# Optimization experiments

Measured on AMD Instinct MI355X. Metric: run time of the kernel, lower is better.

## Reference

```python
import jax, jax.numpy as jnp
import numpy as np

EPS = 1e-8
D = 1024      # embedding_dim
NH = 4        # num_heads
HD = D // NH  # head_dim
B, S = 4, 2048


def setup_inputs() -> dict:
    key = jax.random.key(0)
    k1, k2 = jax.random.split(key)
    x = jax.random.normal(k1, (B, S, 4 * D), dtype=jnp.float32)
    # small-init std = sqrt(2/(5*head_dim)) as in reset_parameters
    std = float(np.sqrt(2.0 / (5.0 * HD)))
    gate_weights = jax.random.normal(k2, (4, NH, HD, HD), dtype=jnp.float32) * std
    # biases: z,i,o zero; f gets powerlaw init (block 0 of 1 -> exponent 0.3)
    term = jnp.arange(HD, dtype=jnp.float32) / (HD - 1.0)
    f_bias = -(-5.0 + 12.0 * term ** 0.3)  # [HD]
    gate_biases = jnp.zeros((4, NH, HD), dtype=jnp.float32)
    gate_biases = gate_biases.at[2].set(jnp.broadcast_to(f_bias, (NH, HD)))
    return {"x_gate_inputs": x, "gate_weights": gate_weights, "gate_biases": gate_biases}


def _slstm_forward(x, W, biases):
    Bn, Sn, _ = x.shape
    # split into 4 gate pre-activations and apply headwise linear per gate
    xg = x.reshape(Bn, Sn, 4, NH, HD)           # gate order z,i,f,o along axis 2
    xg = jnp.moveaxis(xg, 2, 0)                  # [4,B,S,NH,HD]
    # headwise projection: einsum over head-in dim, per gate g and head h
    gates = jnp.einsum('gbshi,ghoi->gbsho', xg, W) + biases[:, None, None]  # [4,B,S,NH,HD]
    gates = jnp.moveaxis(gates, 2, 0)            # [S,4,B,NH,HD] for scan over time

    h0 = jnp.zeros((Bn, NH, HD), dtype=x.dtype)
    carry0 = (h0, h0, h0, jnp.zeros((Bn, NH, HD), dtype=jnp.float32))

    def step(carry, g_t):
        h, c, n, m = carry
        z_b, i_b, f_b, o_b = g_t[0], g_t[1], g_t[2], g_t[3]
        z_val = jnp.tanh(z_b)
        o_val = jax.nn.sigmoid(o_b)
        # faithful to original: exp then log(.+EPS), in m-state dtype (fp32)
        log_f = jnp.log(jnp.exp(f_b).astype(jnp.float32) + EPS)
        log_i = jnp.log(jnp.exp(i_b).astype(jnp.float32) + EPS)
        m_new = jnp.maximum(log_f + m, log_i)
        i_hat = jnp.exp(log_i - m_new).astype(x.dtype)
        f_hat = jnp.exp(log_f + m - m_new).astype(x.dtype)
        c_new = f_hat * c + i_hat * z_val
        n_new = f_hat * n + i_hat
        h_new = o_val * (c_new / (n_new + EPS))
        return (h_new, c_new, n_new, m_new), h_new

    (h_f, c_f, n_f, m_f), hs = jax.lax.scan(step, carry0, gates)
    h_seq = jnp.moveaxis(hs, 0, 1)               # [B,S,NH,HD]
    return h_seq, (h_f, c_f, n_f, m_f)


def reference(x_gate_inputs, gate_weights, gate_biases):
    h_seq, (h_f, c_f, n_f, m_f) = _slstm_forward(x_gate_inputs, gate_weights, gate_biases)
    return h_seq, h_f, c_f, n_f, m_f
```

## Files before the change

kernel.cpp:

```cpp
#include <hip/hip_runtime.h>
#include <cstdint>

#define S_LEN   2048
#define BATCH   4
#define NCH     4096
#define CHUNK   32
#define NCHUNK  64
#define PLANE   ((size_t)S_LEN * NCH)
#define SN      ((size_t)NCHUNK * NCH)
#define EPS     1e-8f

using bf16x8 = __attribute__((ext_vector_type(8))) short;
using u16x8  = __attribute__((ext_vector_type(8))) unsigned short;
using f32x4  = __attribute__((ext_vector_type(4))) float;
typedef unsigned short u16;

__device__ __forceinline__ short f2bf(float f) {
  uint32_t u = __builtin_bit_cast(uint32_t, f);
  u += 0x7fffu + ((u >> 16) & 1u);
  return (short)(u >> 16);
}
__device__ __forceinline__ float bf2f(u16 u) {
  return __builtin_bit_cast(float, (uint32_t)u << 16);
}
__device__ __forceinline__ u16 f2h(float f) {
  _Float16 h = (_Float16)f;
  return __builtin_bit_cast(unsigned short, h);
}
__device__ __forceinline__ float h2f(u16 u) {
  return (float)__builtin_bit_cast(_Float16, u);
}


__global__ __launch_bounds__(1024) void gates_gemm7(
    const float* __restrict__ x, const float* __restrict__ W,
    const float* __restrict__ bias,
    u16* __restrict__ gz16, u16* __restrict__ gi16, u16* __restrict__ gf16,
    u16* __restrict__ go16) {
  __shared__ u16 As[2][16 * 264];

  const int gh  = blockIdx.x;
  const int rg  = blockIdx.y;
  const int g   = gh >> 2, hh = gh & 3;
  const int tid = threadIdx.x;
  const int wave = tid >> 6, lane = tid & 63;
  const int l16 = lane & 15, quad = lane >> 4;
  const int n0  = wave * 16;
  const int row0 = rg * 256;

  bf16x8 Bf[8];
  {
    const float* wp = W + ((size_t)gh << 16) + (n0 + l16) * 256 + quad * 8;
#pragma unroll
    for (int kt = 0; kt < 8; ++kt) {
      float4 w0 = *(const float4*)(wp + kt * 32);
      float4 w1 = *(const float4*)(wp + kt * 32 + 4);
      bf16x8 b;
      b[0] = f2bf(w0.x); b[1] = f2bf(w0.y); b[2] = f2bf(w0.z); b[3] = f2bf(w0.w);
      b[4] = f2bf(w1.x); b[5] = f2bf(w1.y); b[6] = f2bf(w1.z); b[7] = f2bf(w1.w);
      Bf[kt] = b;
    }
  }
  const float bv = bias[gh * 256 + n0 + l16];

  const int sr = tid >> 6, sc = tid & 63;
  const float* sbase = x + (size_t)(row0 + sr) * 4096 + g * 1024 + hh * 256 + sc * 4;

  float4 sreg;
  auto gload = [&](int t) { sreg = *(const float4*)(sbase + (size_t)t * 16 * 4096); };
  auto swrite = [&](int buf) {
    ushort4 u;
    u.x = (u16)f2bf(sreg.x); u.y = (u16)f2bf(sreg.y);
    u.z = (u16)f2bf(sreg.z); u.w = (u16)f2bf(sreg.w);
    *(ushort4*)&As[buf][sr * 264 + sc * 4] = u;
  };

  gload(0); swrite(0);
  __syncthreads();

  for (int t = 0; t < 16; ++t) {
    if (t + 1 < 16) gload(t + 1);

    f32x4 acc = (f32x4){0.f, 0.f, 0.f, 0.f};
#pragma unroll
    for (int kt = 0; kt < 8; ++kt) {
      bf16x8 a = *(const bf16x8*)&As[t & 1][l16 * 264 + kt * 32 + quad * 8];
      acc = __builtin_amdgcn_mfma_f32_16x16x32_bf16(a, Bf[kt], acc, 0, 0, 0);
    }

    {
      int rowb = row0 + t * 16 + quad * 4;
      int sx   = rowb & (S_LEN - 1);
      int bx   = rowb >> 11;
      int ck   = sx >> 5, sin = sx & 31;
      int ch   = bx * 1024 + hh * 256 + n0 + l16;
      size_t idx = ((size_t)ck * NCH + ch) * CHUNK + sin;

      float v0 = acc[0] + bv, v1 = acc[1] + bv, v2 = acc[2] + bv, v3 = acc[3] + bv;
      ushort4 uo;
      if (g == 1) {
        uo.x = f2h(v0); uo.y = f2h(v1); uo.z = f2h(v2); uo.w = f2h(v3);
        *(ushort4*)&gi16[idx] = uo;
      } else if (g == 2) {
        uo.x = f2h(v0); uo.y = f2h(v1); uo.z = f2h(v2); uo.w = f2h(v3);
        *(ushort4*)&gf16[idx] = uo;
      } else if (g == 0) {
        auto tz = [](float v) {
          return (u16)f2bf(1.f - 2.f * __builtin_amdgcn_rcpf(1.f + __expf(2.f * v)));
        };
        uo.x = tz(v0); uo.y = tz(v1); uo.z = tz(v2); uo.w = tz(v3);
        *(ushort4*)&gz16[idx] = uo;
      } else {
        auto sg = [](float v) {
          return (u16)f2bf(__builtin_amdgcn_rcpf(1.f + __expf(-v)));
        };
        uo.x = sg(v0); uo.y = sg(v1); uo.z = sg(v2); uo.w = sg(v3);
        *(ushort4*)&go16[idx] = uo;
      }
    }

    if (t + 1 < 16) {
      swrite((t + 1) & 1);
      __syncthreads();
    }
  }
}

__global__ __launch_bounds__(256) void scan_pass1(
    const u16* __restrict__ gz16, const u16* __restrict__ gi16,
    const u16* __restrict__ gf16, float* __restrict__ sums) {
  const int t  = blockIdx.x * 256 + threadIdx.x;
  const int ch = t & (NCH - 1);
  const int ck = t >> 12;
  const size_t cb = ((size_t)ck * NCH + ch) * CHUNK;

  u16x8 zv[4], iv[4], fv[4];
#pragma unroll
  for (int q = 0; q < 4; ++q) zv[q] = *(const u16x8*)(gz16 + cb + q * 8);
#pragma unroll
  for (int q = 0; q < 4; ++q) iv[q] = *(const u16x8*)(gi16 + cb + q * 8);
#pragma unroll
  for (int q = 0; q < 4; ++q) fv[q] = *(const u16x8*)(gf16 + cb + q * 8);

  float A = 0.f, Bv = -1e30f, D = 0.f, Dn = 0.f;

  auto step = [&](float z, float i, float f) {
    float Bn = fmaxf(Bv + f, i);
    float e1 = __expf(Bv + f - Bn);
    float e2 = __expf(i - Bn);
    D  = e1 * D + e2 * z;
    Dn = e1 * Dn + e2;
    A += f;
    Bv = Bn;
  };

#pragma unroll
  for (int q = 0; q < 4; ++q)
#pragma unroll
    for (int j = 0; j < 8; ++j)
      step(bf2f(zv[q][j]), h2f(iv[q][j]), h2f(fv[q][j]));

  const size_t idx = (size_t)ck * NCH + ch;
  sums[idx]          = A;
  sums[SN + idx]     = Bv;
  sums[2 * SN + idx] = D;
  sums[3 * SN + idx] = Dn;
}

__global__ __launch_bounds__(256) void scan_pass2(
    const float* __restrict__ sums, float* __restrict__ ent) {
  const int gt   = blockIdx.x * 256 + threadIdx.x;
  const int ch   = gt >> 6;
  const int lane = gt & 63;

  const size_t idx = (size_t)lane * NCH + ch;
  float A = sums[idx];
  float B = sums[SN + idx];
  float D = sums[2 * SN + idx];
  float N = sums[3 * SN + idx];

#pragma unroll
  for (int d = 1; d < 64; d <<= 1) {
    float A1 = __shfl_up(A, d, 64);
    float B1 = __shfl_up(B, d, 64);
    float D1 = __shfl_up(D, d, 64);
    float N1 = __shfl_up(N, d, 64);
    if (lane >= d) {
      float Bn = fmaxf(B1 + A, B);
      float e1 = __expf(B1 + A - Bn);
      float e2 = __expf(B - Bn);
      D = e1 * D1 + e2 * D;
      N = e1 * N1 + e2 * N;
      A = A + A1;
      B = Bn;
    }
  }

  float Ae = __shfl_up(A, 1, 64);
  float Be = __shfl_up(B, 1, 64);
  float De = __shfl_up(D, 1, 64);
  float Ne = __shfl_up(N, 1, 64);

  float c, n, m;
  if (lane == 0) {
    c = 0.f; n = 0.f; m = 0.f;
  } else {
    m = fmaxf(Ae, Be);
    float eb = __expf(Be - m);
    c = eb * De;
    n = eb * Ne;
  }

  ent[idx]          = c;
  ent[SN + idx]     = n;
  ent[2 * SN + idx] = m;
}

__global__ __launch_bounds__(256) void scan_pass3(
    const u16* __restrict__ gz16, const u16* __restrict__ gi16,
    const u16* __restrict__ gf16, const u16* __restrict__ go16,
    const float* __restrict__ ent, float* __restrict__ out) {
  const int t  = blockIdx.x * 256 + threadIdx.x;
  const int ch = t & (NCH - 1);
  const int ck = t >> 12;
  const size_t cb = ((size_t)ck * NCH + ch) * CHUNK;

  u16x8 zv[4], iv[4], fv[4], ov[4];
#pragma unroll
  for (int q = 0; q < 4; ++q) zv[q] = *(const u16x8*)(gz16 + cb + q * 8);
#pragma unroll
  for (int q = 0; q < 4; ++q) iv[q] = *(const u16x8*)(gi16 + cb + q * 8);
#pragma unroll
  for (int q = 0; q < 4; ++q) fv[q] = *(const u16x8*)(gf16 + cb + q * 8);
#pragma unroll
  for (int q = 0; q < 4; ++q) ov[q] = *(const u16x8*)(go16 + cb + q * 8);

  const size_t idx0 = (size_t)ck * NCH + ch;
  float c = ent[idx0];
  float n = ent[SN + idx0];
  float m = ent[2 * SN + idx0];

  const int b = ch >> 10, d = ch & 1023;
  float* hout = out + (size_t)b * (S_LEN * 1024) + (size_t)(ck * CHUNK) * 1024 + d;

  float hv = 0.f;
#pragma unroll
  for (int q = 0; q < 4; ++q) {
#pragma unroll
    for (int j = 0; j < 8; ++j) {
      float z = bf2f(zv[q][j]);
      float i = h2f(iv[q][j]);
      float f = h2f(fv[q][j]);
      float o = bf2f(ov[q][j]);
      float mn = fmaxf(f + m, i);
      float fh = __expf(f + m - mn);
      float ih = __expf(i - mn);
      c = fh * c + ih * z;
      n = fh * n + ih;
      m = mn;
      hv = o * c * __builtin_amdgcn_rcpf(n + EPS);
      hout[(size_t)(q * 8 + j) * 1024] = hv;
    }
  }

  if (ck == NCHUNK - 1) {
    float* fin = out + (size_t)BATCH * S_LEN * 1024;
    fin[ch]            = hv;
    fin[NCH + ch]      = c;
    fin[2 * NCH + ch]  = n;
    fin[3 * NCH + ch]  = m;
  }
}

extern "C" void kernel_launch(void* const* d_in, const int* in_sizes, int n_in,
                              void* d_out, int out_size, void* d_ws, size_t ws_size,
                              hipStream_t stream) {
  const float* x    = (const float*)d_in[0];
  const float* W    = (const float*)d_in[1];
  const float* bias = (const float*)d_in[2];
  float* out = (float*)d_out;

  u16*   gz16 = (u16*)d_ws;
  u16*   gi16 = gz16 + PLANE;
  u16*   gf16 = gi16 + PLANE;
  u16*   go16 = gf16 + PLANE;
  float* sums = (float*)(go16 + PLANE);
  float* ent  = sums + 4 * SN;

  gates_gemm7<<<dim3(16, 32), dim3(1024), 0, stream>>>(x, W, bias, gz16, gi16, gf16, go16);
  scan_pass1<<<dim3(1024), dim3(256), 0, stream>>>(gz16, gi16, gf16, sums);
  scan_pass2<<<dim3(1024), dim3(256), 0, stream>>>(sums, ent);
  scan_pass3<<<dim3(1024), dim3(256), 0, stream>>>(gz16, gi16, gf16, go16, ent, out);
}
```

Before: 274.7 us.

## Fuse three-pass chunked scan into one kernel using shared memory

Merges the three scan kernels (chunk reduce, cross-chunk prefix, chunk apply) into a single kernel. Each 1024-thread block owns 16 channels across all 64 chunks and passes chunk summaries through shared memory instead of global workspace. This removes two launches, the global round-trips for sums and entry states, and the reload of z/i/f gates, which now stay in registers. The trade-off is a lower block count (256 blocks of 1024 threads), so more registers are live per thread and occupancy may drop. The global loads in the first phase also become strided, since 16 channels times 64 B each fall within one slot.

```diff
diff --git a/kernel.cpp b/kernel.cpp
--- a/kernel.cpp
+++ b/kernel.cpp
@@ -7,7 +7,6 @@
 #define CHUNK   32
 #define NCHUNK  64
 #define PLANE   ((size_t)S_LEN * NCH)
-#define SN      ((size_t)NCHUNK * NCH)
 #define EPS     1e-8f
 
 using bf16x8 = __attribute__((ext_vector_type(8))) short;
@@ -126,149 +125,137 @@
   }
 }
 
-__global__ __launch_bounds__(256) void scan_pass1(
-    const u16* __restrict__ gz16, const u16* __restrict__ gi16,
-    const u16* __restrict__ gf16, float* __restrict__ sums) {
-  const int t  = blockIdx.x * 256 + threadIdx.x;
-  const int ch = t & (NCH - 1);
-  const int ck = t >> 12;
-  const size_t cb = ((size_t)ck * NCH + ch) * CHUNK;
-
-  u16x8 zv[4], iv[4], fv[4];
-#pragma unroll
-  for (int q = 0; q < 4; ++q) zv[q] = *(const u16x8*)(gz16 + cb + q * 8);
-#pragma unroll
-  for (int q = 0; q < 4; ++q) iv[q] = *(const u16x8*)(gi16 + cb + q * 8);
-#pragma unroll
-  for (int q = 0; q < 4; ++q) fv[q] = *(const u16x8*)(gf16 + cb + q * 8);
-
-  float A = 0.f, Bv = -1e30f, D = 0.f, Dn = 0.f;
-
-  auto step = [&](float z, float i, float f) {
-    float Bn = fmaxf(Bv + f, i);
-    float e1 = __expf(Bv + f - Bn);
-    float e2 = __expf(i - Bn);
-    D  = e1 * D + e2 * z;
-    Dn = e1 * Dn + e2;
-    A += f;
-    Bv = Bn;
-  };
-
-#pragma unroll
-  for (int q = 0; q < 4; ++q)
-#pragma unroll
-    for (int j = 0; j < 8; ++j)
-      step(bf2f(zv[q][j]), h2f(iv[q][j]), h2f(fv[q][j]));
-
-  const size_t idx = (size_t)ck * NCH + ch;
-  sums[idx]          = A;
-  sums[SN + idx]     = Bv;
-  sums[2 * SN + idx] = D;
-  sums[3 * SN + idx] = Dn;
-}
-
-__global__ __launch_bounds__(256) void scan_pass2(
-    const float* __restrict__ sums, float* __restrict__ ent) {
-  const int gt   = blockIdx.x * 256 + threadIdx.x;
-  const int ch   = gt >> 6;
-  const int lane = gt & 63;
-
-  const size_t idx = (size_t)lane * NCH + ch;
-  float A = sums[idx];
-  float B = sums[SN + idx];
-  float D = sums[2 * SN + idx];
-  float N = sums[3 * SN + idx];
-
-#pragma unroll
-  for (int d = 1; d < 64; d <<= 1) {
-    float A1 = __shfl_up(A, d, 64);
-    float B1 = __shfl_up(B, d, 64);
-    float D1 = __shfl_up(D, d, 64);
-    float N1 = __shfl_up(N, d, 64);
-    if (lane >= d) {
-      float Bn = fmaxf(B1 + A, B);
-      float e1 = __expf(B1 + A - Bn);
-      float e2 = __expf(B - Bn);
-      D = e1 * D1 + e2 * D;
-      N = e1 * N1 + e2 * N;
-      A = A + A1;
-      B = Bn;
-    }
-  }
-
-  float Ae = __shfl_up(A, 1, 64);
-  float Be = __shfl_up(B, 1, 64);
-  float De = __shfl_up(D, 1, 64);
-  float Ne = __shfl_up(N, 1, 64);
-
-  float c, n, m;
-  if (lane == 0) {
-    c = 0.f; n = 0.f; m = 0.f;
-  } else {
-    m = fmaxf(Ae, Be);
-    float eb = __expf(Be - m);
-    c = eb * De;
-    n = eb * Ne;
-  }
-
-  ent[idx]          = c;
-  ent[SN + idx]     = n;
-  ent[2 * SN + idx] = m;
-}
-
-__global__ __launch_bounds__(256) void scan_pass3(
+__global__ __launch_bounds__(1024) void scan_fused(
     const u16* __restrict__ gz16, const u16* __restrict__ gi16,
     const u16* __restrict__ gf16, const u16* __restrict__ go16,
-    const float* __restrict__ ent, float* __restrict__ out) {
-  const int t  = blockIdx.x * 256 + threadIdx.x;
-  const int ch = t & (NCH - 1);
-  const int ck = t >> 12;
-  const size_t cb = ((size_t)ck * NCH + ch) * CHUNK;
-
-  u16x8 zv[4], iv[4], fv[4], ov[4];
+    float* __restrict__ out) {
+  __shared__ float sA[64][17], sB[64][17], sD[64][17], sN[64][17];
+
+  const int tid = threadIdx.x;
+  const int ch_local = tid & 15;
+  const int slot     = tid >> 4;
+  const int ch       = blockIdx.x * 16 + ch_local;
+  const size_t cb    = ((size_t)slot * NCH + ch) * CHUNK;
+
+  u16x8 zv[4], iv[4], fv[4];
 #pragma unroll
   for (int q = 0; q < 4; ++q) zv[q] = *(const u16x8*)(gz16 + cb + q * 8);
 #pragma unroll
   for (int q = 0; q < 4; ++q) iv[q] = *(const u16x8*)(gi16 + cb + q * 8);
 #pragma unroll
   for (int q = 0; q < 4; ++q) fv[q] = *(const u16x8*)(gf16 + cb + q * 8);
-#pragma unroll
-  for (int q = 0; q < 4; ++q) ov[q] = *(const u16x8*)(go16 + cb + q * 8);
-
-  const size_t idx0 = (size_t)ck * NCH + ch;
-  float c = ent[idx0];
-  float n = ent[SN + idx0];
-  float m = ent[2 * SN + idx0];
-
-  const int b = ch >> 10, d = ch & 1023;
-  float* hout = out + (size_t)b * (S_LEN * 1024) + (size_t)(ck * CHUNK) * 1024 + d;
-
-  float hv = 0.f;
-#pragma unroll
-  for (int q = 0; q < 4; ++q) {
-#pragma unroll
-    for (int j = 0; j < 8; ++j) {
-      float z = bf2f(zv[q][j]);
-      float i = h2f(iv[q][j]);
-      float f = h2f(fv[q][j]);
-      float o = bf2f(ov[q][j]);
-      float mn = fmaxf(f + m, i);
-      float fh = __expf(f + m - mn);
-      float ih = __expf(i - mn);
-      c = fh * c + ih * z;
-      n = fh * n + ih;
-      m = mn;
-      hv = o * c * __builtin_amdgcn_rcpf(n + EPS);
-      hout[(size_t)(q * 8 + j) * 1024] = hv;
-    }
-  }
-
-  if (ck == NCHUNK - 1) {
-    float* fin = out + (size_t)BATCH * S_LEN * 1024;
-    fin[ch]            = hv;
-    fin[NCH + ch]      = c;
-    fin[2 * NCH + ch]  = n;
-    fin[3 * NCH + ch]  = m;
+
+  {
+    float A = 0.f, Bv = -1e30f, D = 0.f, Dn = 0.f;
+#pragma unroll
+    for (int q = 0; q < 4; ++q) {
+#pragma unroll
+      for (int j = 0; j < 8; ++j) {
+        float z = bf2f(zv[q][j]);
+        float i = h2f(iv[q][j]);
+        float f = h2f(fv[q][j]);
+        float Bn = fmaxf(Bv + f, i);
+        float e1 = __expf(Bv + f - Bn);
+        float e2 = __expf(i - Bn);
+        D  = e1 * D + e2 * z;
+        Dn = e1 * Dn + e2;
+        A += f;
+        Bv = Bn;
+      }
+    }
+    sA[slot][ch_local] = A;
+    sB[slot][ch_local] = Bv;
+    sD[slot][ch_local] = D;
+    sN[slot][ch_local] = Dn;
+  }
+  __syncthreads();
+
+  {
+    const int w    = tid >> 6;
+    const int lane = tid & 63;
+
+    float A = sA[lane][w];
+    float B = sB[lane][w];
+    float D = sD[lane][w];
+    float N = sN[lane][w];
+
+#pragma unroll
+    for (int d = 1; d < 64; d <<= 1) {
+      float A1 = __shfl_up(A, d, 64);
+      float B1 = __shfl_up(B, d, 64);
+      float D1 = __shfl_up(D, d, 64);
+      float N1 = __shfl_up(N, d, 64);
+      if (lane >= d) {
+        float Bn = fmaxf(B1 + A, B);
+        float e1 = __expf(B1 + A - Bn);
+        float e2 = __expf(B - Bn);
+        D = e1 * D1 + e2 * D;
+        N = e1 * N1 + e2 * N;
+        A = A + A1;
+        B = Bn;
+      }
+    }
+
+    float Ae = __shfl_up(A, 1, 64);
+    float Be = __shfl_up(B, 1, 64);
+    float De = __shfl_up(D, 1, 64);
+    float Ne = __shfl_up(N, 1, 64);
+
+    float c, n, m;
+    if (lane == 0) {
+      c = 0.f; n = 0.f; m = 0.f;
+    } else {
+      m = fmaxf(Ae, Be);
+      float eb = __expf(Be - m);
+      c = eb * De;
+      n = eb * Ne;
+    }
+
+    sA[lane][w] = c;
+    sB[lane][w] = n;
+    sD[lane][w] = m;
+  }
+  __syncthreads();
+
+  {
+    float c = sA[slot][ch_local];
+    float n = sB[slot][ch_local];
+    float m = sD[slot][ch_local];
+
+    u16x8 ov[4];
+#pragma unroll
+    for (int q = 0; q < 4; ++q) ov[q] = *(const u16x8*)(go16 + cb + q * 8);
+
+    const int b = ch >> 10, d = ch & 1023;
+    float* hout = out + (size_t)b * (S_LEN * 1024) + (size_t)(slot * CHUNK) * 1024 + d;
+
+    float hv = 0.f;
+#pragma unroll
+    for (int q = 0; q < 4; ++q) {
+#pragma unroll
+      for (int j = 0; j < 8; ++j) {
+        float z = bf2f(zv[q][j]);
+        float i = h2f(iv[q][j]);
+        float f = h2f(fv[q][j]);
+        float o = bf2f(ov[q][j]);
+        float mn = fmaxf(f + m, i);
+        float fh = __expf(f + m - mn);
+        float ih = __expf(i - mn);
+        c = fh * c + ih * z;
+        n = fh * n + ih;
+        m = mn;
+        hv = o * c * __builtin_amdgcn_rcpf(n + EPS);
+        hout[(size_t)(q * 8 + j) * 1024] = hv;
+      }
+    }
+
+    if (slot == NCHUNK - 1) {
+      float* fin = out + (size_t)BATCH * S_LEN * 1024;
+      fin[ch]            = hv;
+      fin[NCH + ch]      = c;
+      fin[2 * NCH + ch]  = n;
+      fin[3 * NCH + ch]  = m;
+    }
   }
 }
 
@@ -284,11 +271,7 @@
   u16*   gi16 = gz16 + PLANE;
   u16*   gf16 = gi16 + PLANE;
   u16*   go16 = gf16 + PLANE;
-  float* sums = (float*)(go16 + PLANE);
-  float* ent  = sums + 4 * SN;
 
   gates_gemm7<<<dim3(16, 32), dim3(1024), 0, stream>>>(x, W, bias, gz16, gi16, gf16, go16);
-  scan_pass1<<<dim3(1024), dim3(256), 0, stream>>>(gz16, gi16, gf16, sums);
-  scan_pass2<<<dim3(1024), dim3(256), 0, stream>>>(sums, ent);
-  scan_pass3<<<dim3(1024), dim3(256), 0, stream>>>(gz16, gi16, gf16, go16, ent, out);
-}
+  scan_fused<<<dim3(256), dim3(1024), 0, stream>>>(gz16, gi16, gf16, go16, out);
+}
```

Measured after the change: 250.1 us. 8.9% less time.
